# Kernel optimization log

Hardware: AMD Instinct MI355X
Metric: run time of the kernel (lower is better)

The kernel has to match this reference:

```python
import jax, jax.numpy as jnp
import numpy as np
from math import gcd

KAISER_BETA = 5.0  # scipy resample_poly default window=('kaiser', 5.0)


def _firwin_kaiser(numtaps, cutoff, beta):
    # lowpass firwin equivalent: windowed-sinc, normalized to unity DC gain
    m = np.arange(numtaps) - (numtaps - 1) / 2.0
    h = cutoff * np.sinc(cutoff * m)
    h *= np.kaiser(numtaps, beta)
    h /= h.sum()
    return h


def _output_len(len_h, in_len, up, down):
    # full upfirdn output length
    return ((in_len - 1) * up + len_h - 1) // down + 1


def _make_filter(du, su, n_in):
    # replicates scipy.signal.resample_poly filter design + zero padding
    g = gcd(su, du)
    up, down = su // g, du // g
    max_rate = max(up, down)
    half_len = 10 * max_rate
    h = _firwin_kaiser(2 * half_len + 1, 1.0 / max_rate, KAISER_BETA) * up
    n_pre_pad = down - half_len % down
    n_out = n_in * up // down + bool((n_in * up) % down)
    n_pre_remove = (half_len + n_pre_pad) // down
    n_post_pad = 0
    while _output_len(len(h) + n_pre_pad + n_post_pad, n_in, up, down) < n_out + n_pre_remove:
        n_post_pad += 1
    h = np.concatenate([np.zeros(n_pre_pad), h, np.zeros(n_post_pad)]).astype(np.float32)
    return h


B, T, C = 16, 1_280_000, 4


def setup_inputs() -> dict:
    key = jax.random.key(0)
    x = jax.random.normal(key, (B, T, C), dtype=jnp.float32)
    h = jnp.asarray(_make_filter(640, 50, T))  # [1345]
    return {"x": x, "h": h, "su": 50, "du": 640}


def reference(x, h, su, du):
    # polyphase resampling: upsample by `up` (lhs_dilation), FIR filter h
    # (full convolution), downsample by `down` (stride) == scipy upfirdn,
    # then trim transients exactly as scipy.signal.resample_poly does.
    Bx, Tx, Cx = x.shape
    g = gcd(su, du)
    up, down = su // g, du // g  # 5, 64
    half_len = 10 * max(up, down)
    n_pre_pad = down - half_len % down
    n_pre_remove = (half_len + n_pre_pad) // down
    n_out = Tx * up // down + bool((Tx * up) % down)
    K = h.shape[0]
    # resample along time axis (axis=1): [B, T, C] -> [B*C, 1, T]
    xc = jnp.transpose(x, (0, 2, 1)).reshape(Bx * Cx, 1, Tx)
    kern = h[::-1].reshape(1, 1, K).astype(x.dtype)  # flip: conv, not corr
    y = jax.lax.conv_general_dilated(
        xc, kern,
        window_strides=(down,),
        padding=[(K - 1, K - 1)],
        lhs_dilation=(up,),
        dimension_numbers=("NCH", "OIH", "NCH"),
    )  # [B*C, 1, L_full]
    y = y[:, 0, n_pre_remove:n_pre_remove + n_out]
    return jnp.transpose(y.reshape(Bx, Cx, n_out), (0, 2, 1))  # [B, n_out, C]
```

## Files before the change

kernel.cpp:

```cpp
#include <hip/hip_runtime.h>

typedef _Float16 h2 __attribute__((ext_vector_type(2)));
typedef _Float16 h4 __attribute__((ext_vector_type(4)));

#define T_IN   1280000
#define N_OUT  100000
#define NQ     20000
#define KH     1345
#define NMP    176
#define QT     64
#define NTILE  313
#define OFFJ   159
#define NPAIR  2240
#define PLANE  9216
#define SWZ(b) ((b) ^ ((((b) >> 7) & 15) << 3))
#define PKRTZ(a, b) __builtin_bit_cast(h2, __builtin_amdgcn_cvt_pkrtz((a), (b)))

__global__ void build_tables(const float* __restrict__ h, unsigned* __restrict__ ws) {
    int m = blockIdx.x * blockDim.x + threadIdx.x;
    if (m >= NMP) return;
    #pragma unroll
    for (int r = 0; r < 5; ++r) {
        int ilo = 5 * (2 * m)     - 256 + 64 * r;
        int ihi = 5 * (2 * m + 1) - 256 + 64 * r;
        float vlo = (ilo >= 0 && ilo < KH) ? h[ilo] : 0.f;
        float vhi = (ihi >= 0 && ihi < KH) ? h[ihi] : 0.f;
        h2 p = PKRTZ(vhi, vlo);
        ws[m * 5 + r] = __builtin_bit_cast(unsigned, p);
    }
}

#define DOT_R(AR, TH, TL) \
  AR.x = __builtin_amdgcn_fdot2(TH, Xl0, AR.x, false); \
  AR.x = __builtin_amdgcn_fdot2(TL, Xh0, AR.x, false); \
  AR.y = __builtin_amdgcn_fdot2(TH, Xl1, AR.y, false); \
  AR.y = __builtin_amdgcn_fdot2(TL, Xh1, AR.y, false); \
  AR.z = __builtin_amdgcn_fdot2(TH, Xl2, AR.z, false); \
  AR.z = __builtin_amdgcn_fdot2(TL, Xh2, AR.z, false); \
  AR.w = __builtin_amdgcn_fdot2(TH, Xl3, AR.w, false); \
  AR.w = __builtin_amdgcn_fdot2(TL, Xh3, AR.w, false);

__launch_bounds__(512, 8)
__global__ void downsample_poly(const float* __restrict__ x,
                                const unsigned* __restrict__ ws,
                                float* __restrict__ out) {
    __shared__ __align__(16) char lds[40960];
    const int tid = threadIdx.x;
    const int b   = blockIdx.y;
    const int q0  = blockIdx.x * QT;
    const int jlo = 64 * q0 - OFFJ;
    const float4* __restrict__ xb = (const float4*)x + (size_t)b * T_IN;

    #pragma unroll
    for (int it = 0; it < 5; ++it) {
        int i2 = tid + it * 512;
        if (i2 < NPAIR) {
            int j0 = jlo + 2 * i2;
            float4 v0 = make_float4(0.f, 0.f, 0.f, 0.f), v1 = v0;
            if ((unsigned)j0       < (unsigned)T_IN) v0 = xb[j0];
            if ((unsigned)(j0 + 1) < (unsigned)T_IN) v1 = xb[j0 + 1];
            int bb = SWZ(4 * i2);
            *(h2*)(lds + bb)             = PKRTZ(v0.x, v1.x);
            *(h2*)(lds + bb +     PLANE) = PKRTZ(v0.y, v1.y);
            *(h2*)(lds + bb + 2 * PLANE) = PKRTZ(v0.z, v1.z);
            *(h2*)(lds + bb + 3 * PLANE) = PKRTZ(v0.w, v1.w);
        }
    }
    __syncthreads();

    const int dq = tid & 63;
    const int su = __builtin_amdgcn_readfirstlane(tid >> 6);
    float4 a0 = make_float4(0.f,0.f,0.f,0.f), a1 = a0, a2 = a0, a3 = a0, a4 = a0;
    const int rb0 = 128 * dq + 696 - 88 * su;

    #pragma unroll 2
    for (int g = 0; g < 11; ++g) {
        int sw = SWZ(rb0 - 8 * g);
        h4 X0 = *(const h4*)(lds + sw);
        h4 X1 = *(const h4*)(lds + sw +     PLANE);
        h4 X2 = *(const h4*)(lds + sw + 2 * PLANE);
        h4 X3 = *(const h4*)(lds + sw + 3 * PLANE);
        h2 Xl0 = {X0[0], X0[1]}, Xh0 = {X0[2], X0[3]};
        h2 Xl1 = {X1[0], X1[1]}, Xh1 = {X1[2], X1[3]};
        h2 Xl2 = {X2[0], X2[1]}, Xh2 = {X2[2], X2[3]};
        h2 Xl3 = {X3[0], X3[1]}, Xh3 = {X3[2], X3[3]};
        const unsigned* tw = ws + (110 * su + 10 * g);
        h2 th, tl;
        th = __builtin_bit_cast(h2, tw[5]); tl = __builtin_bit_cast(h2, tw[0]); DOT_R(a0, th, tl)
        th = __builtin_bit_cast(h2, tw[6]); tl = __builtin_bit_cast(h2, tw[1]); DOT_R(a1, th, tl)
        th = __builtin_bit_cast(h2, tw[7]); tl = __builtin_bit_cast(h2, tw[2]); DOT_R(a2, th, tl)
        th = __builtin_bit_cast(h2, tw[8]); tl = __builtin_bit_cast(h2, tw[3]); DOT_R(a3, th, tl)
        th = __builtin_bit_cast(h2, tw[9]); tl = __builtin_bit_cast(h2, tw[4]); DOT_R(a4, th, tl)
    }

    __syncthreads();
    {
        float4* pp = (float4*)(lds + tid * 80);
        pp[0] = a0; pp[1] = a1; pp[2] = a2; pp[3] = a3; pp[4] = a4;
    }
    __syncthreads();
    if (tid < 320 && 5 * q0 + tid < 5 * NQ) {
        float sx = 0.f, sy = 0.f, sz = 0.f, sw2 = 0.f;
        #pragma unroll
        for (int ss = 0; ss < 8; ++ss) {
            float4 p = *(const float4*)(lds + ss * 5120 + tid * 16);
            sx += p.x; sy += p.y; sz += p.z; sw2 += p.w;
        }
        ((float4*)out)[(size_t)b * N_OUT + 5 * (size_t)q0 + tid] =
            make_float4(sx, sy, sz, sw2);
    }
}

extern "C" void kernel_launch(void* const* d_in, const int* in_sizes, int n_in,
                              void* d_out, int out_size, void* d_ws, size_t ws_size,
                              hipStream_t stream) {
    const float* x = (const float*)d_in[0];
    const float* h = (const float*)d_in[1];
    float* out = (float*)d_out;
    unsigned* ws = (unsigned*)d_ws;

    hipLaunchKernelGGL(build_tables, dim3(1), dim3(192), 0, stream, h, ws);
    hipLaunchKernelGGL(downsample_poly, dim3(NTILE, 16), dim3(512), 0, stream,
                       x, ws, out);
}
```

Baseline: 449.5 us.

## Make downsample kernel persistent with double-buffered LDS and register prefetch

Replaces the one-tile-per-block grid with a persistent grid of 512 blocks that loop over all batch×tile tasks. The next task's input is prefetched into registers while the current tile's dot products run, and LDS is double-buffered so the load latency can overlap compute. The costs are 80KB of dynamic LDS per block, lower occupancy (launch bounds go from 8 to 4 waves per SIMD hint), extra registers for the prefetch, and possible tail imbalance since 5008 tasks do not divide evenly over 512 blocks.

New measurement: 459.2 us. +2.1%, slower.

```diff
diff --git a/kernel.cpp b/kernel.cpp
--- a/kernel.cpp
+++ b/kernel.cpp
@@ -8,11 +8,14 @@
 #define NQ     20000
 #define KH     1345
 #define NMP    176
-#define QT     64
 #define NTILE  313
+#define NTASK  5008
+#define GRID   512
 #define OFFJ   159
 #define NPAIR  2240
 #define PLANE  9216
+#define SLOT   40960
+#define LDSSZ  81920
 #define SWZ(b) ((b) ^ ((((b) >> 7) & 15) << 3))
 #define PKRTZ(a, b) __builtin_bit_cast(h2, __builtin_amdgcn_cvt_pkrtz((a), (b)))
 
@@ -40,74 +43,100 @@
   AR.w = __builtin_amdgcn_fdot2(TH, Xl3, AR.w, false); \
   AR.w = __builtin_amdgcn_fdot2(TL, Xh3, AR.w, false);
 
-__launch_bounds__(512, 8)
+#define LOAD_P(VA, VB, P) \
+    { int i2 = tid + (P) * 512; \
+      int j0 = jlo_ + 2 * i2; \
+      VA = make_float4(0.f, 0.f, 0.f, 0.f); VB = VA; \
+      if (i2 < NPAIR) { \
+          if ((unsigned)j0       < (unsigned)T_IN) VA = xb_[j0]; \
+          if ((unsigned)(j0 + 1) < (unsigned)T_IN) VB = xb_[j0 + 1]; \
+      } }
+
+#define LOAD_TASK(UU) \
+    { int bb_ = (UU) / NTILE; \
+      int tt_ = (UU) - bb_ * NTILE; \
+      const float4* __restrict__ xb_ = (const float4*)x + (size_t)bb_ * T_IN; \
+      int jlo_ = (tt_ << 12) - OFFJ; \
+      LOAD_P(va0, vb0, 0) LOAD_P(va1, vb1, 1) LOAD_P(va2, vb2, 2) \
+      LOAD_P(va3, vb3, 3) LOAD_P(va4, vb4, 4) }
+
+#define WR_P(VA, VB, P) \
+    { int i2 = tid + (P) * 512; \
+      if (i2 < NPAIR) { \
+          int bb = SWZ(4 * i2); \
+          *(h2*)(buf + bb)             = PKRTZ(VA.x, VB.x); \
+          *(h2*)(buf + bb +     PLANE) = PKRTZ(VA.y, VB.y); \
+          *(h2*)(buf + bb + 2 * PLANE) = PKRTZ(VA.z, VB.z); \
+          *(h2*)(buf + bb + 3 * PLANE) = PKRTZ(VA.w, VB.w); } }
+
+__launch_bounds__(512, 4)
 __global__ void downsample_poly(const float* __restrict__ x,
                                 const unsigned* __restrict__ ws,
                                 float* __restrict__ out) {
-    __shared__ __align__(16) char lds[40960];
+    extern __shared__ __align__(16) char lds[];
     const int tid = threadIdx.x;
-    const int b   = blockIdx.y;
-    const int q0  = blockIdx.x * QT;
-    const int jlo = 64 * q0 - OFFJ;
-    const float4* __restrict__ xb = (const float4*)x + (size_t)b * T_IN;
-
-    #pragma unroll
-    for (int it = 0; it < 5; ++it) {
-        int i2 = tid + it * 512;
-        if (i2 < NPAIR) {
-            int j0 = jlo + 2 * i2;
-            float4 v0 = make_float4(0.f, 0.f, 0.f, 0.f), v1 = v0;
-            if ((unsigned)j0       < (unsigned)T_IN) v0 = xb[j0];
-            if ((unsigned)(j0 + 1) < (unsigned)T_IN) v1 = xb[j0 + 1];
-            int bb = SWZ(4 * i2);
-            *(h2*)(lds + bb)             = PKRTZ(v0.x, v1.x);
-            *(h2*)(lds + bb +     PLANE) = PKRTZ(v0.y, v1.y);
-            *(h2*)(lds + bb + 2 * PLANE) = PKRTZ(v0.z, v1.z);
-            *(h2*)(lds + bb + 3 * PLANE) = PKRTZ(v0.w, v1.w);
-        }
-    }
-    __syncthreads();
-
-    const int dq = tid & 63;
-    const int su = __builtin_amdgcn_readfirstlane(tid >> 6);
-    float4 a0 = make_float4(0.f,0.f,0.f,0.f), a1 = a0, a2 = a0, a3 = a0, a4 = a0;
+    const int dq  = tid & 63;
+    const int su  = __builtin_amdgcn_readfirstlane(tid >> 6);
     const int rb0 = 128 * dq + 696 - 88 * su;
 
-    #pragma unroll 2
-    for (int g = 0; g < 11; ++g) {
-        int sw = SWZ(rb0 - 8 * g);
-        h4 X0 = *(const h4*)(lds + sw);
-        h4 X1 = *(const h4*)(lds + sw +     PLANE);
-        h4 X2 = *(const h4*)(lds + sw + 2 * PLANE);
-        h4 X3 = *(const h4*)(lds + sw + 3 * PLANE);
-        h2 Xl0 = {X0[0], X0[1]}, Xh0 = {X0[2], X0[3]};
-        h2 Xl1 = {X1[0], X1[1]}, Xh1 = {X1[2], X1[3]};
-        h2 Xl2 = {X2[0], X2[1]}, Xh2 = {X2[2], X2[3]};
-        h2 Xl3 = {X3[0], X3[1]}, Xh3 = {X3[2], X3[3]};
-        const unsigned* tw = ws + (110 * su + 10 * g);
-        h2 th, tl;
-        th = __builtin_bit_cast(h2, tw[5]); tl = __builtin_bit_cast(h2, tw[0]); DOT_R(a0, th, tl)
-        th = __builtin_bit_cast(h2, tw[6]); tl = __builtin_bit_cast(h2, tw[1]); DOT_R(a1, th, tl)
-        th = __builtin_bit_cast(h2, tw[7]); tl = __builtin_bit_cast(h2, tw[2]); DOT_R(a2, th, tl)
-        th = __builtin_bit_cast(h2, tw[8]); tl = __builtin_bit_cast(h2, tw[3]); DOT_R(a3, th, tl)
-        th = __builtin_bit_cast(h2, tw[9]); tl = __builtin_bit_cast(h2, tw[4]); DOT_R(a4, th, tl)
-    }
+    float4 va0, va1, va2, va3, va4, vb0, vb1, vb2, vb3, vb4;
 
-    __syncthreads();
-    {
-        float4* pp = (float4*)(lds + tid * 80);
-        pp[0] = a0; pp[1] = a1; pp[2] = a2; pp[3] = a3; pp[4] = a4;
-    }
-    __syncthreads();
-    if (tid < 320 && 5 * q0 + tid < 5 * NQ) {
-        float sx = 0.f, sy = 0.f, sz = 0.f, sw2 = 0.f;
-        #pragma unroll
-        for (int ss = 0; ss < 8; ++ss) {
-            float4 p = *(const float4*)(lds + ss * 5120 + tid * 16);
-            sx += p.x; sy += p.y; sz += p.z; sw2 += p.w;
+    int u = blockIdx.x;
+    int parity = 0;
+    LOAD_TASK(u);
+
+    for (; u < NTASK; u += GRID, parity ^= 1) {
+        char* buf = lds + parity * SLOT;
+
+        WR_P(va0, vb0, 0) WR_P(va1, vb1, 1) WR_P(va2, vb2, 2)
+        WR_P(va3, vb3, 3) WR_P(va4, vb4, 4)
+        __syncthreads();
+
+        int un = u + GRID;
+        if (un >= NTASK) un = u;
+        LOAD_TASK(un);
+
+        float4 a0 = make_float4(0.f,0.f,0.f,0.f), a1 = a0, a2 = a0, a3 = a0, a4 = a0;
+        #pragma unroll 2
+        for (int g = 0; g < 11; ++g) {
+            int sw = SWZ(rb0 - 8 * g);
+            h4 X0 = *(const h4*)(buf + sw);
+            h4 X1 = *(const h4*)(buf + sw +     PLANE);
+            h4 X2 = *(const h4*)(buf + sw + 2 * PLANE);
+            h4 X3 = *(const h4*)(buf + sw + 3 * PLANE);
+            h2 Xl0 = {X0[0], X0[1]}, Xh0 = {X0[2], X0[3]};
+            h2 Xl1 = {X1[0], X1[1]}, Xh1 = {X1[2], X1[3]};
+            h2 Xl2 = {X2[0], X2[1]}, Xh2 = {X2[2], X2[3]};
+            h2 Xl3 = {X3[0], X3[1]}, Xh3 = {X3[2], X3[3]};
+            const unsigned* tw = ws + (110 * su + 10 * g);
+            h2 th, tl;
+            th = __builtin_bit_cast(h2, tw[5]); tl = __builtin_bit_cast(h2, tw[0]); DOT_R(a0, th, tl)
+            th = __builtin_bit_cast(h2, tw[6]); tl = __builtin_bit_cast(h2, tw[1]); DOT_R(a1, th, tl)
+            th = __builtin_bit_cast(h2, tw[7]); tl = __builtin_bit_cast(h2, tw[2]); DOT_R(a2, th, tl)
+            th = __builtin_bit_cast(h2, tw[8]); tl = __builtin_bit_cast(h2, tw[3]); DOT_R(a3, th, tl)
+            th = __builtin_bit_cast(h2, tw[9]); tl = __builtin_bit_cast(h2, tw[4]); DOT_R(a4, th, tl)
         }
-        ((float4*)out)[(size_t)b * N_OUT + 5 * (size_t)q0 + tid] =
-            make_float4(sx, sy, sz, sw2);
+
+        __syncthreads();
+        {
+            float4* pp = (float4*)(buf + tid * 80);
+            pp[0] = a0; pp[1] = a1; pp[2] = a2; pp[3] = a3; pp[4] = a4;
+        }
+        __syncthreads();
+        {
+            int bcu = u / NTILE;
+            int q0  = (u - bcu * NTILE) << 6;
+            if (tid < 320 && 5 * q0 + tid < 5 * NQ) {
+                float sx = 0.f, sy = 0.f, sz = 0.f, sw2 = 0.f;
+                #pragma unroll
+                for (int ss = 0; ss < 8; ++ss) {
+                    float4 p = *(const float4*)(buf + ss * 5120 + tid * 16);
+                    sx += p.x; sy += p.y; sz += p.z; sw2 += p.w;
+                }
+                ((float4*)out)[(size_t)bcu * N_OUT + 5 * (size_t)q0 + tid] =
+                    make_float4(sx, sy, sz, sw2);
+            }
+        }
     }
 }
 
@@ -119,7 +148,10 @@
     float* out = (float*)d_out;
     unsigned* ws = (unsigned*)d_ws;
 
+    hipFuncSetAttribute((const void*)downsample_poly,
+                        hipFuncAttributeMaxDynamicSharedMemorySize, LDSSZ);
+
     hipLaunchKernelGGL(build_tables, dim3(1), dim3(192), 0, stream, h, ws);
-    hipLaunchKernelGGL(downsample_poly, dim3(NTILE, 16), dim3(512), 0, stream,
+    hipLaunchKernelGGL(downsample_poly, dim3(GRID), dim3(512), LDSSZ, stream,
                        x, ws, out);
 }
```
